# Performance work log

Measured on AMD Instinct MI355X. Metric: run time of the kernel, lower is better.

The kernel has to match this reference:

```python
import jax, jax.numpy as jnp
import numpy as np
import math

NUM_HEADS = 16
D_MODEL = 1024
HEAD_DIM = D_MODEL // NUM_HEADS


def setup_inputs() -> dict:
    key = jax.random.key(0)
    k1, k2, k3 = jax.random.split(key, 3)
    x = jax.random.normal(k1, (4, 2048, D_MODEL), dtype=jnp.float32)
    # Linear(d_model, 3*d_model, bias=False): y = x @ w_qkv, w_qkv: [d_model, 3*d_model]
    w_qkv = jax.random.normal(k2, (D_MODEL, 3 * D_MODEL), dtype=jnp.float32) * (1.0 / math.sqrt(D_MODEL))
    w_o = jax.random.normal(k3, (D_MODEL, D_MODEL), dtype=jnp.float32) * (1.0 / math.sqrt(D_MODEL))
    return {"x": x, "w_qkv": w_qkv, "w_o": w_o}


def reference(x, w_qkv, w_o):
    B, S, _ = x.shape
    H, Dh = NUM_HEADS, HEAD_DIM
    qkv = (x @ w_qkv).reshape(B, S, 3, H, Dh)
    q = qkv[:, :, 0].transpose(0, 2, 1, 3)  # [B, H, S, Dh]
    k = qkv[:, :, 1].transpose(0, 2, 1, 3)
    v = qkv[:, :, 2].transpose(0, 2, 1, 3)
    scale = 1.0 / math.sqrt(Dh + 1e-9)
    scores = jnp.einsum("bhqd,bhkd->bhqk", q, k) * scale  # [B, H, S, S]
    probs = jax.nn.softmax(scores, axis=-1)
    # dropout is identity in eval mode
    out = jnp.einsum("bhqk,bhkd->bhqd", probs, v)  # [B, H, S, Dh]
    out = out.transpose(0, 2, 1, 3).reshape(B, S, H * Dh)
    return out @ w_o
```

## Files before the change

kernel.cpp:

```cpp
#include <hip/hip_runtime.h>
#include <hip/hip_bf16.h>

typedef __bf16 bf16_t;
typedef __bf16 bf16x8 __attribute__((ext_vector_type(8)));
typedef float f32x4 __attribute__((ext_vector_type(4)));
typedef unsigned int uint32x2 __attribute__((ext_vector_type(2)));
typedef unsigned int uint32x4 __attribute__((ext_vector_type(4)));

#define B_SZ 4
#define SEQ 2048
#define NH 16
#define DH 64
#define DM 1024

__device__ __forceinline__ void gload_lds16(const bf16_t* g, bf16_t* l) {
  __builtin_amdgcn_global_load_lds(
      (const __attribute__((address_space(1))) unsigned int*)g,
      (__attribute__((address_space(3))) unsigned int*)l, 16, 0, 0);
}

__device__ __forceinline__ unsigned lds_b32addr(void* p) {
  return (unsigned)(uintptr_t)(__attribute__((address_space(3))) void*)p;
}

__global__ __launch_bounds__(256) void f32_to_bf16_kernel(
    const float* __restrict__ in, bf16_t* __restrict__ out, int n) {
  int i = (blockIdx.x * blockDim.x + threadIdx.x) * 4;
  if (i >= n) return;
  float4 v = *reinterpret_cast<const float4*>(in + i);
  bf16_t o[4] = {(bf16_t)v.x, (bf16_t)v.y, (bf16_t)v.z, (bf16_t)v.w};
  *reinterpret_cast<uint2*>(out + i) = *reinterpret_cast<const uint2*>(o);
}

__global__ __launch_bounds__(256) void transpose_f32_bf16_kernel(
    const float* __restrict__ in, bf16_t* __restrict__ outT, int K, int N) {
  __shared__ float tile[32][33];
  const int tx = threadIdx.x & 31;
  const int ty = threadIdx.x >> 5;
  const int n0 = blockIdx.x * 32;
  const int k0 = blockIdx.y * 32;
#pragma unroll
  for (int j = 0; j < 4; ++j)
    tile[ty + j * 8][tx] = in[(size_t)(k0 + ty + j * 8) * N + n0 + tx];
  __syncthreads();
#pragma unroll
  for (int j = 0; j < 4; ++j)
    outT[(size_t)(n0 + ty + j * 8) * K + k0 + tx] = (bf16_t)tile[tx][ty + j * 8];
}

template <typename OutT>
__global__ __launch_bounds__(256) void gemm_bt_kernel(
    const bf16_t* __restrict__ A, const bf16_t* __restrict__ Bt,
    OutT* __restrict__ C, int M, int N, int K) {
  __shared__ __align__(16) bf16_t As[128 * 64];
  __shared__ __align__(16) bf16_t Bs[128 * 64];

  const int tid = threadIdx.x;
  const int lane = tid & 63;
  const int wid = tid >> 6;
  const int l16 = lane & 15;
  const int g4 = lane >> 4;
  const int m0 = blockIdx.y * 128;
  const int n0 = blockIdx.x * 128;
  const int wm = (wid >> 1) * 64;
  const int wn = (wid & 1) * 64;

  const int srow = wid * 8 + (lane >> 3);
  const int scol = (lane & 7) * 8;
  const bf16_t* ap = A + (size_t)(m0 + srow) * K + scol;
  const bf16_t* bp = Bt + (size_t)(n0 + srow) * K + scol;

  f32x4 acc[4][4] = {};

  for (int k0 = 0; k0 < K; k0 += 64) {
    __syncthreads();
#pragma unroll
    for (int t = 0; t < 4; ++t) {
      gload_lds16(ap + k0 + (size_t)t * 32 * K, &As[(t * 32 + wid * 8) * 64]);
      gload_lds16(bp + k0 + (size_t)t * 32 * K, &Bs[(t * 32 + wid * 8) * 64]);
    }
    __syncthreads();

#pragma unroll
    for (int ks = 0; ks < 2; ++ks) {
      bf16x8 af[4], bfm[4];
#pragma unroll
      for (int i = 0; i < 4; ++i)
        af[i] = *reinterpret_cast<const bf16x8*>(
            &As[(wm + i * 16 + l16) * 64 + ks * 32 + g4 * 8]);
#pragma unroll
      for (int i = 0; i < 4; ++i)
        bfm[i] = *reinterpret_cast<const bf16x8*>(
            &Bs[(wn + i * 16 + l16) * 64 + ks * 32 + g4 * 8]);
#pragma unroll
      for (int mi = 0; mi < 4; ++mi)
#pragma unroll
        for (int ni = 0; ni < 4; ++ni)
          acc[mi][ni] = __builtin_amdgcn_mfma_f32_16x16x32_bf16(
              af[mi], bfm[ni], acc[mi][ni], 0, 0, 0);
    }
  }

#pragma unroll
  for (int mi = 0; mi < 4; ++mi)
#pragma unroll
    for (int ni = 0; ni < 4; ++ni)
#pragma unroll
      for (int r = 0; r < 4; ++r) {
        int row = m0 + wm + mi * 16 + g4 * 4 + r;
        int col = n0 + wn + ni * 16 + l16;
        C[(size_t)row * N + col] = (OutT)acc[mi][ni][r];
      }
}

__global__ __launch_bounds__(256) void attn_kernel(
    const bf16_t* __restrict__ qkv, bf16_t* __restrict__ out) {
  __shared__ __align__(16) unsigned char smem[18432];
  bf16_t* Vlds = (bf16_t*)smem;
  float(*Obuf)[66] = (float(*)[66])smem;
  float* lbuf = (float*)(smem + 16896);

  const int tid = threadIdx.x;
  const int lane = tid & 63;
  const int wid = tid >> 6;
  const int l16 = lane & 15;
  const int g4 = lane >> 4;

  const int D = blockIdx.x;
  const int g = ((D >> 8) << 3) + (D & 7);
  const int h = g & 15;
  const int b = g >> 4;
  const int q0 = ((D >> 3) & 31) * 64;

  const int RS = 3 * DM;
  const size_t base = (size_t)b * SEQ * RS;

  bf16x8 qf[4][2];
#pragma unroll
  for (int qb = 0; qb < 4; ++qb)
#pragma unroll
    for (int kh = 0; kh < 2; ++kh)
      qf[qb][kh] = __builtin_bit_cast(
          bf16x8, *reinterpret_cast<const uint4*>(
                      qkv + base + (size_t)(q0 + qb * 16 + l16) * RS + h * DH +
                      kh * 32 + g4 * 8));

  const bf16_t* kbase =
      qkv + base + (size_t)(wid * 16 + l16) * RS + DM + h * DH + g4 * 8;

  const int keyoff = ((lane >> 5) << 6) + wid * 16 + (((lane >> 3) & 3) << 2) +
                     ((lane >> 1) & 3);
  const bf16_t* vsrc =
      qkv + base + (size_t)keyoff * RS + 2 * DM + h * DH + (lane & 1) * 8;
  bf16_t* vwave = Vlds + wid * 2048;
  const unsigned vlane = lds_b32addr(vwave) + (lane << 3);

  f32x4 acc_o[16] = {};
  float lsum[4] = {0.f, 0.f, 0.f, 0.f};
  const float c_exp2 = 0.18033688011112042f;

  for (int k0 = 0; k0 < SEQ; k0 += 128) {
    const bf16_t* vs = vsrc + (size_t)k0 * RS;
#pragma unroll
    for (int t = 0; t < 4; ++t)
      gload_lds16(vs + t * 16, vwave + t * 512);

    bf16x8 kf[2][2];
#pragma unroll
    for (int half = 0; half < 2; ++half)
#pragma unroll
      for (int kh = 0; kh < 2; ++kh)
        kf[half][kh] = __builtin_bit_cast(
            bf16x8, *reinterpret_cast<const uint4*>(
                        kbase + (size_t)(k0 + half * 64) * RS + kh * 32));

    asm volatile("s_waitcnt vmcnt(0)" ::: "memory");

    uint32x2 vr[4][2];
#pragma unroll
    for (int db = 0; db < 4; ++db)
#pragma unroll
      for (int eh = 0; eh < 2; ++eh) {
        unsigned a = vlane + db * 1024 + eh * 512;
        asm volatile("ds_read_b64_tr_b16 %0, %1"
                     : "=v"(vr[db][eh])
                     : "v"(a));
      }
    asm volatile("s_waitcnt lgkmcnt(0)" ::: "memory");
    __builtin_amdgcn_sched_barrier(0);

    bf16x8 vf[4];
#pragma unroll
    for (int db = 0; db < 4; ++db) {
      uint32x4 c = {vr[db][0].x, vr[db][0].y, vr[db][1].x, vr[db][1].y};
      vf[db] = __builtin_bit_cast(bf16x8, c);
    }

    f32x4 sA[4] = {}, sB[4] = {};
#pragma unroll
    for (int qb = 0; qb < 4; ++qb) {
      sA[qb] = __builtin_amdgcn_mfma_f32_16x16x32_bf16(kf[0][0], qf[qb][0], sA[qb], 0, 0, 0);
      sA[qb] = __builtin_amdgcn_mfma_f32_16x16x32_bf16(kf[0][1], qf[qb][1], sA[qb], 0, 0, 0);
      sB[qb] = __builtin_amdgcn_mfma_f32_16x16x32_bf16(kf[1][0], qf[qb][0], sB[qb], 0, 0, 0);
      sB[qb] = __builtin_amdgcn_mfma_f32_16x16x32_bf16(kf[1][1], qf[qb][1], sB[qb], 0, 0, 0);
    }

    bf16x8 pf[4];
#pragma unroll
    for (int qb = 0; qb < 4; ++qb) {
      float p0 = exp2f(sA[qb][0] * c_exp2);
      float p1 = exp2f(sA[qb][1] * c_exp2);
      float p2 = exp2f(sA[qb][2] * c_exp2);
      float p3 = exp2f(sA[qb][3] * c_exp2);
      float p4 = exp2f(sB[qb][0] * c_exp2);
      float p5 = exp2f(sB[qb][1] * c_exp2);
      float p6 = exp2f(sB[qb][2] * c_exp2);
      float p7 = exp2f(sB[qb][3] * c_exp2);
      lsum[qb] += ((p0 + p1) + (p2 + p3)) + ((p4 + p5) + (p6 + p7));
      pf[qb][0] = (bf16_t)p0; pf[qb][1] = (bf16_t)p1;
      pf[qb][2] = (bf16_t)p2; pf[qb][3] = (bf16_t)p3;
      pf[qb][4] = (bf16_t)p4; pf[qb][5] = (bf16_t)p5;
      pf[qb][6] = (bf16_t)p6; pf[qb][7] = (bf16_t)p7;
    }

#pragma unroll
    for (int qb = 0; qb < 4; ++qb)
#pragma unroll
      for (int db = 0; db < 4; ++db)
        acc_o[qb * 4 + db] = __builtin_amdgcn_mfma_f32_16x16x32_bf16(
            pf[qb], vf[db], acc_o[qb * 4 + db], 0, 0, 0);
  }

#pragma unroll
  for (int qb = 0; qb < 4; ++qb) {
    float t = lsum[qb];
    t += __shfl_xor(t, 16, 64);
    t += __shfl_xor(t, 32, 64);
    if (g4 == 0) lbuf[wid * 64 + qb * 16 + l16] = t;
  }

  for (int ph = 0; ph < 4; ++ph) {
    __syncthreads();
    if (wid == ph) {
#pragma unroll
      for (int qb = 0; qb < 4; ++qb)
#pragma unroll
        for (int db = 0; db < 4; ++db)
#pragma unroll
          for (int r = 0; r < 4; ++r) {
            int q = qb * 16 + g4 * 4 + r;
            int d = db * 16 + l16;
            if (ph == 0)
              Obuf[q][d] = acc_o[qb * 4 + db][r];
            else
              Obuf[q][d] += acc_o[qb * 4 + db][r];
          }
    }
  }
  __syncthreads();

  {
    int q = wid * 16 + l16;
    float l = lbuf[0 * 64 + q] + lbuf[1 * 64 + q] + lbuf[2 * 64 + q] +
              lbuf[3 * 64 + q];
    float inv = 1.f / l;
    bf16_t ob[16];
#pragma unroll
    for (int c = 0; c < 16; ++c)
      ob[c] = (bf16_t)(Obuf[q][g4 * 16 + c] * inv);
    bf16_t* op = out + (size_t)(b * SEQ + q0 + q) * DM + h * DH + g4 * 16;
    *reinterpret_cast<uint4*>(op) = *reinterpret_cast<const uint4*>(&ob[0]);
    *reinterpret_cast<uint4*>(op + 8) = *reinterpret_cast<const uint4*>(&ob[8]);
  }
}

extern "C" void kernel_launch(void* const* d_in, const int* in_sizes, int n_in,
                              void* d_out, int out_size, void* d_ws, size_t ws_size,
                              hipStream_t stream) {
  const float* x = (const float*)d_in[0];
  const float* w_qkv = (const float*)d_in[1];
  const float* w_o = (const float*)d_in[2];
  float* out = (float*)d_out;

  bf16_t* xb = (bf16_t*)d_ws;
  bf16_t* wqkvt = xb + (size_t)8192 * 1024;
  bf16_t* wot = wqkvt + (size_t)3072 * 1024;
  bf16_t* qkv = wot + (size_t)1024 * 1024;
  bf16_t* attn = qkv + (size_t)8192 * 3072;

  dim3 blk(256);

  f32_to_bf16_kernel<<<8192, blk, 0, stream>>>(x, xb, 8192 * 1024);
  transpose_f32_bf16_kernel<<<dim3(3072 / 32, 1024 / 32), blk, 0, stream>>>(
      w_qkv, wqkvt, 1024, 3072);
  transpose_f32_bf16_kernel<<<dim3(1024 / 32, 1024 / 32), blk, 0, stream>>>(
      w_o, wot, 1024, 1024);

  gemm_bt_kernel<bf16_t><<<dim3(3072 / 128, 8192 / 128), blk, 0, stream>>>(
      xb, wqkvt, qkv, 8192, 3072, 1024);
  attn_kernel<<<2048, blk, 0, stream>>>(qkv, attn);
  gemm_bt_kernel<float><<<dim3(1024 / 128, 8192 / 128), blk, 0, stream>>>(
      attn, wot, out, 8192, 1024, 1024);
}
```

Before: 259.8 us.

## Double-buffer V tiles in attention and fold softmax scale into Q weights

The attention loop now double-buffers V in LDS, prefetching the next 128-key V tile via global_load_lds while the current tile is computed, with counted vmcnt waits instead of a full drain. The softmax scale times log2(e) is folded into the Q columns of the transposed QKV weight, so the inner loop uses the raw exp2 intrinsic without a multiply. This doubles the attention LDS footprint and changes bf16 rounding of Q slightly.

Measured after the change: 233.6 us. -10.1%, faster.

```diff
diff --git a/kernel.cpp b/kernel.cpp
--- a/kernel.cpp
+++ b/kernel.cpp
@@ -12,6 +12,7 @@
 #define NH 16
 #define DH 64
 #define DM 1024
+#define RSQ (3 * DM)
 
 __device__ __forceinline__ void gload_lds16(const bf16_t* g, bf16_t* l) {
   __builtin_amdgcn_global_load_lds(
@@ -33,7 +34,8 @@
 }
 
 __global__ __launch_bounds__(256) void transpose_f32_bf16_kernel(
-    const float* __restrict__ in, bf16_t* __restrict__ outT, int K, int N) {
+    const float* __restrict__ in, bf16_t* __restrict__ outT, int K, int N,
+    int scale_cols, float scale) {
   __shared__ float tile[32][33];
   const int tx = threadIdx.x & 31;
   const int ty = threadIdx.x >> 5;
@@ -44,8 +46,11 @@
     tile[ty + j * 8][tx] = in[(size_t)(k0 + ty + j * 8) * N + n0 + tx];
   __syncthreads();
 #pragma unroll
-  for (int j = 0; j < 4; ++j)
-    outT[(size_t)(n0 + ty + j * 8) * K + k0 + tx] = (bf16_t)tile[tx][ty + j * 8];
+  for (int j = 0; j < 4; ++j) {
+    int n = n0 + ty + j * 8;
+    float s = (n < scale_cols) ? scale : 1.0f;
+    outT[(size_t)n * K + k0 + tx] = (bf16_t)(tile[tx][ty + j * 8] * s);
+  }
 }
 
 template <typename OutT>
@@ -113,12 +118,101 @@
       }
 }
 
+template <bool PRE>
+__device__ __forceinline__ void attn_body(
+    const bf16_t* kp, const bf16_t* vp_next, bf16_t* vst_next, unsigned vrd,
+    const bf16x8 (&qf)[4][2], f32x4 (&acc_o)[16], float (&lsum)[4]) {
+  uint32x4 kf[2][2];
+#pragma unroll
+  for (int half = 0; half < 2; ++half)
+#pragma unroll
+    for (int kh = 0; kh < 2; ++kh)
+      asm volatile("global_load_dwordx4 %0, %1, off"
+                   : "=v"(kf[half][kh])
+                   : "v"(kp + (size_t)half * 64 * RSQ + kh * 32)
+                   : "memory");
+
+  if constexpr (PRE) {
+#pragma unroll
+    for (int t = 0; t < 4; ++t)
+      gload_lds16(vp_next + t * 16, vst_next + t * 512);
+  }
+
+  if constexpr (PRE)
+    asm volatile("s_waitcnt vmcnt(8)" ::: "memory");
+  else
+    asm volatile("s_waitcnt vmcnt(4)" ::: "memory");
+
+  uint32x2 vr[4][2];
+#define TRR(dst, OFFSTR)                              \
+  asm volatile("ds_read_b64_tr_b16 %0, %1 offset:" OFFSTR \
+               : "=v"(dst)                            \
+               : "v"(vrd))
+  TRR(vr[0][0], "0");    TRR(vr[0][1], "512");
+  TRR(vr[1][0], "1024"); TRR(vr[1][1], "1536");
+  TRR(vr[2][0], "2048"); TRR(vr[2][1], "2560");
+  TRR(vr[3][0], "3072"); TRR(vr[3][1], "3584");
+#undef TRR
+
+  if constexpr (PRE)
+    asm volatile("s_waitcnt vmcnt(4)" ::: "memory");
+  else
+    asm volatile("s_waitcnt vmcnt(0)" ::: "memory");
+  __builtin_amdgcn_sched_barrier(0);
+
+  f32x4 sA[4] = {}, sB[4] = {};
+#pragma unroll
+  for (int qb = 0; qb < 4; ++qb) {
+    sA[qb] = __builtin_amdgcn_mfma_f32_16x16x32_bf16(
+        __builtin_bit_cast(bf16x8, kf[0][0]), qf[qb][0], sA[qb], 0, 0, 0);
+    sA[qb] = __builtin_amdgcn_mfma_f32_16x16x32_bf16(
+        __builtin_bit_cast(bf16x8, kf[0][1]), qf[qb][1], sA[qb], 0, 0, 0);
+    sB[qb] = __builtin_amdgcn_mfma_f32_16x16x32_bf16(
+        __builtin_bit_cast(bf16x8, kf[1][0]), qf[qb][0], sB[qb], 0, 0, 0);
+    sB[qb] = __builtin_amdgcn_mfma_f32_16x16x32_bf16(
+        __builtin_bit_cast(bf16x8, kf[1][1]), qf[qb][1], sB[qb], 0, 0, 0);
+  }
+
+  bf16x8 pf[4];
+#pragma unroll
+  for (int qb = 0; qb < 4; ++qb) {
+    float p0 = __builtin_amdgcn_exp2f(sA[qb][0]);
+    float p1 = __builtin_amdgcn_exp2f(sA[qb][1]);
+    float p2 = __builtin_amdgcn_exp2f(sA[qb][2]);
+    float p3 = __builtin_amdgcn_exp2f(sA[qb][3]);
+    float p4 = __builtin_amdgcn_exp2f(sB[qb][0]);
+    float p5 = __builtin_amdgcn_exp2f(sB[qb][1]);
+    float p6 = __builtin_amdgcn_exp2f(sB[qb][2]);
+    float p7 = __builtin_amdgcn_exp2f(sB[qb][3]);
+    lsum[qb] += ((p0 + p1) + (p2 + p3)) + ((p4 + p5) + (p6 + p7));
+    pf[qb][0] = (bf16_t)p0; pf[qb][1] = (bf16_t)p1;
+    pf[qb][2] = (bf16_t)p2; pf[qb][3] = (bf16_t)p3;
+    pf[qb][4] = (bf16_t)p4; pf[qb][5] = (bf16_t)p5;
+    pf[qb][6] = (bf16_t)p6; pf[qb][7] = (bf16_t)p7;
+  }
+
+  asm volatile("s_waitcnt lgkmcnt(0)" ::: "memory");
+  __builtin_amdgcn_sched_barrier(0);
+  bf16x8 vf[4];
+#pragma unroll
+  for (int db = 0; db < 4; ++db) {
+    uint32x4 c = {vr[db][0].x, vr[db][0].y, vr[db][1].x, vr[db][1].y};
+    vf[db] = __builtin_bit_cast(bf16x8, c);
+  }
+#pragma unroll
+  for (int qb = 0; qb < 4; ++qb)
+#pragma unroll
+    for (int db = 0; db < 4; ++db)
+      acc_o[qb * 4 + db] = __builtin_amdgcn_mfma_f32_16x16x32_bf16(
+          pf[qb], vf[db], acc_o[qb * 4 + db], 0, 0, 0);
+}
+
 __global__ __launch_bounds__(256) void attn_kernel(
     const bf16_t* __restrict__ qkv, bf16_t* __restrict__ out) {
-  __shared__ __align__(16) unsigned char smem[18432];
+  __shared__ __align__(16) unsigned char smem[33792];
   bf16_t* Vlds = (bf16_t*)smem;
   float(*Obuf)[66] = (float(*)[66])smem;
-  float* lbuf = (float*)(smem + 16896);
+  float* lbuf = (float*)(smem + 32768);
 
   const int tid = threadIdx.x;
   const int lane = tid & 63;
@@ -132,8 +226,7 @@
   const int b = g >> 4;
   const int q0 = ((D >> 3) & 31) * 64;
 
-  const int RS = 3 * DM;
-  const size_t base = (size_t)b * SEQ * RS;
+  const size_t base = (size_t)b * SEQ * RSQ;
 
   bf16x8 qf[4][2];
 #pragma unroll
@@ -142,94 +235,34 @@
     for (int kh = 0; kh < 2; ++kh)
       qf[qb][kh] = __builtin_bit_cast(
           bf16x8, *reinterpret_cast<const uint4*>(
-                      qkv + base + (size_t)(q0 + qb * 16 + l16) * RS + h * DH +
+                      qkv + base + (size_t)(q0 + qb * 16 + l16) * RSQ + h * DH +
                       kh * 32 + g4 * 8));
 
   const bf16_t* kbase =
-      qkv + base + (size_t)(wid * 16 + l16) * RS + DM + h * DH + g4 * 8;
+      qkv + base + (size_t)(wid * 16 + l16) * RSQ + DM + h * DH + g4 * 8;
 
   const int keyoff = ((lane >> 5) << 6) + wid * 16 + (((lane >> 3) & 3) << 2) +
                      ((lane >> 1) & 3);
   const bf16_t* vsrc =
-      qkv + base + (size_t)keyoff * RS + 2 * DM + h * DH + (lane & 1) * 8;
-  bf16_t* vwave = Vlds + wid * 2048;
+      qkv + base + (size_t)keyoff * RSQ + 2 * DM + h * DH + (lane & 1) * 8;
+  bf16_t* vwave = Vlds + wid * 4096;
   const unsigned vlane = lds_b32addr(vwave) + (lane << 3);
 
   f32x4 acc_o[16] = {};
   float lsum[4] = {0.f, 0.f, 0.f, 0.f};
-  const float c_exp2 = 0.18033688011112042f;
-
-  for (int k0 = 0; k0 < SEQ; k0 += 128) {
-    const bf16_t* vs = vsrc + (size_t)k0 * RS;
-#pragma unroll
-    for (int t = 0; t < 4; ++t)
-      gload_lds16(vs + t * 16, vwave + t * 512);
-
-    bf16x8 kf[2][2];
-#pragma unroll
-    for (int half = 0; half < 2; ++half)
-#pragma unroll
-      for (int kh = 0; kh < 2; ++kh)
-        kf[half][kh] = __builtin_bit_cast(
-            bf16x8, *reinterpret_cast<const uint4*>(
-                        kbase + (size_t)(k0 + half * 64) * RS + kh * 32));
-
-    asm volatile("s_waitcnt vmcnt(0)" ::: "memory");
-
-    uint32x2 vr[4][2];
-#pragma unroll
-    for (int db = 0; db < 4; ++db)
-#pragma unroll
-      for (int eh = 0; eh < 2; ++eh) {
-        unsigned a = vlane + db * 1024 + eh * 512;
-        asm volatile("ds_read_b64_tr_b16 %0, %1"
-                     : "=v"(vr[db][eh])
-                     : "v"(a));
-      }
-    asm volatile("s_waitcnt lgkmcnt(0)" ::: "memory");
-    __builtin_amdgcn_sched_barrier(0);
-
-    bf16x8 vf[4];
-#pragma unroll
-    for (int db = 0; db < 4; ++db) {
-      uint32x4 c = {vr[db][0].x, vr[db][0].y, vr[db][1].x, vr[db][1].y};
-      vf[db] = __builtin_bit_cast(bf16x8, c);
-    }
-
-    f32x4 sA[4] = {}, sB[4] = {};
-#pragma unroll
-    for (int qb = 0; qb < 4; ++qb) {
-      sA[qb] = __builtin_amdgcn_mfma_f32_16x16x32_bf16(kf[0][0], qf[qb][0], sA[qb], 0, 0, 0);
-      sA[qb] = __builtin_amdgcn_mfma_f32_16x16x32_bf16(kf[0][1], qf[qb][1], sA[qb], 0, 0, 0);
-      sB[qb] = __builtin_amdgcn_mfma_f32_16x16x32_bf16(kf[1][0], qf[qb][0], sB[qb], 0, 0, 0);
-      sB[qb] = __builtin_amdgcn_mfma_f32_16x16x32_bf16(kf[1][1], qf[qb][1], sB[qb], 0, 0, 0);
-    }
-
-    bf16x8 pf[4];
-#pragma unroll
-    for (int qb = 0; qb < 4; ++qb) {
-      float p0 = exp2f(sA[qb][0] * c_exp2);
-      float p1 = exp2f(sA[qb][1] * c_exp2);
-      float p2 = exp2f(sA[qb][2] * c_exp2);
-      float p3 = exp2f(sA[qb][3] * c_exp2);
-      float p4 = exp2f(sB[qb][0] * c_exp2);
-      float p5 = exp2f(sB[qb][1] * c_exp2);
-      float p6 = exp2f(sB[qb][2] * c_exp2);
-      float p7 = exp2f(sB[qb][3] * c_exp2);
-      lsum[qb] += ((p0 + p1) + (p2 + p3)) + ((p4 + p5) + (p6 + p7));
-      pf[qb][0] = (bf16_t)p0; pf[qb][1] = (bf16_t)p1;
-      pf[qb][2] = (bf16_t)p2; pf[qb][3] = (bf16_t)p3;
-      pf[qb][4] = (bf16_t)p4; pf[qb][5] = (bf16_t)p5;
-      pf[qb][6] = (bf16_t)p6; pf[qb][7] = (bf16_t)p7;
-    }
-
-#pragma unroll
-    for (int qb = 0; qb < 4; ++qb)
-#pragma unroll
-      for (int db = 0; db < 4; ++db)
-        acc_o[qb * 4 + db] = __builtin_amdgcn_mfma_f32_16x16x32_bf16(
-            pf[qb], vf[db], acc_o[qb * 4 + db], 0, 0, 0);
-  }
+
+#pragma unroll
+  for (int t = 0; t < 4; ++t) gload_lds16(vsrc + t * 16, vwave + t * 512);
+
+  for (int i = 0; i < 15; ++i) {
+    const bf16_t* kp = kbase + (size_t)i * 128 * RSQ;
+    const bf16_t* vp_next = vsrc + (size_t)(i + 1) * 128 * RSQ;
+    bf16_t* vst_next = vwave + ((i + 1) & 1) * 2048;
+    unsigned vrd = vlane + (i & 1) * 4096;
+    attn_body<true>(kp, vp_next, vst_next, vrd, qf, acc_o, lsum);
+  }
+  attn_body<false>(kbase + (size_t)15 * 128 * RSQ, nullptr, nullptr,
+                   vlane + 4096, qf, acc_o, lsum);
 
 #pragma unroll
   for (int qb = 0; qb < 4; ++qb) {
@@ -289,12 +322,13 @@
   bf16_t* attn = qkv + (size_t)8192 * 3072;
 
   dim3 blk(256);
+  const float c_exp2 = 0.18033688011112042f;
 
   f32_to_bf16_kernel<<<8192, blk, 0, stream>>>(x, xb, 8192 * 1024);
   transpose_f32_bf16_kernel<<<dim3(3072 / 32, 1024 / 32), blk, 0, stream>>>(
-      w_qkv, wqkvt, 1024, 3072);
+      w_qkv, wqkvt, 1024, 3072, 1024, c_exp2);
   transpose_f32_bf16_kernel<<<dim3(1024 / 32, 1024 / 32), blk, 0, stream>>>(
-      w_o, wot, 1024, 1024);
+      w_o, wot, 1024, 1024, 0, 1.0f);
 
   gemm_bt_kernel<bf16_t><<<dim3(3072 / 128, 8192 / 128), blk, 0, stream>>>(
       xb, wqkvt, qkv, 8192, 3072, 1024);
```
